# Performance work log

Measured on AMD Instinct MI355X. Metric: run time of the kernel, lower is better.

Reference implementation:

```python
import jax, jax.numpy as jnp
import numpy as np

WINDOW_SIZE = 100  # band half-width = WINDOW_SIZE // 2 = 50, inclusive


def setup_inputs() -> dict:
    key = jax.random.key(0)
    kq, kk, kv = jax.random.split(key, 3)
    shape = (2, 8, 4096, 64)  # [B, H, S, D]
    return {
        "query": jax.random.normal(kq, shape, dtype=jnp.float32),
        "key": jax.random.normal(kk, shape, dtype=jnp.float32),
        "value": jax.random.normal(kv, shape, dtype=jnp.float32),
    }


def reference(query, key, value):
    B, H, S, D = query.shape
    half = WINDOW_SIZE // 2
    scale = 1.0 / jnp.sqrt(jnp.asarray(D, dtype=jnp.float32))
    # Full dense scores (faithful to the original module): [B, H, S, S]
    scores = jnp.einsum("bhqd,bhkd->bhqk", query, key) * scale
    # Sliding-window band mask: row i attends to j in [i-half, i+half]
    idx = jnp.arange(S)
    band = jnp.abs(idx[:, None] - idx[None, :]) <= half  # [S, S]
    scores = jnp.where(band[None, None, :, :], scores, -jnp.inf)
    attn = jax.nn.softmax(scores, axis=-1)
    attn = jnp.nan_to_num(attn, nan=0.0)  # matches torch.nan_to_num(w, 0.0)
    return jnp.einsum("bhqk,bhkd->bhqd", attn, value)
```

## Files before the change

### kernel.cpp

```cpp
#include <hip/hip_runtime.h>

#define S_LEN 4096
#define DIM   64
#define HALF  50
#define RB    256
#define WQ    16
#define THREADS 1024
#define KCAP  384
#define SCALE 0.125f

typedef __attribute__((ext_vector_type(8))) short bf16x8;
typedef __attribute__((ext_vector_type(4))) float f32x4;

__device__ __forceinline__ unsigned int bf16_rne(float f) {
    unsigned int u = __float_as_uint(f);
    return (u + 0x7fffu + ((u >> 16) & 1u)) >> 16;
}
__device__ __forceinline__ unsigned int pk2(float lo, float hi) {
    return bf16_rne(lo) | (bf16_rne(hi) << 16);
}
__device__ __forceinline__ bf16x8 cvt8(float4 a, float4 b) {
    uint4 t = make_uint4(pk2(a.x, a.y), pk2(a.z, a.w), pk2(b.x, b.y), pk2(b.z, b.w));
    return __builtin_bit_cast(bf16x8, t);
}

__global__ __launch_bounds__(THREADS, 4)
void lattn_mfma(const float* __restrict__ Q, const float* __restrict__ K,
                const float* __restrict__ V, float* __restrict__ O) {
    __shared__ unsigned short Ks[KCAP * 64];
    __shared__ unsigned short Vs[DIM * KCAP];
    __shared__ unsigned short Ps[16 * 16 * 40];

    const int nwg = gridDim.x;
    const int cpx = nwg >> 3;
    const int bid = blockIdx.x;
    const int logical = (bid & 7) * cpx + (bid >> 3);
    const int bh = logical >> 4;
    const int r0 = (logical & 15) * RB;

    const size_t base = (size_t)bh * (S_LEN * DIM);
    const float* Qg = Q + base;
    const float* Kg = K + base;
    const float* Vg = V + base;
    float*       Og = O + base;

    const int kstart = (r0 >= HALF) ? ((r0 - HALF) & ~31) : 0;
    const int kend   = min(S_LEN, r0 + RB + HALF);

    const int u = threadIdx.x;
    const int lane = u & 63;
    const int wv_  = u >> 6;
    const int g  = lane >> 4;
    const int cc = lane & 15;
    const int qlo = r0 + WQ * wv_;

    float4 kA[3], kB[3];
    float4 vA[2][4];
    float4 qA[2], qB[2];

    #pragma unroll
    for (int i = 0; i < 3; ++i) {
        const int kg  = kstart + (u >> 3) + i * 128;
        const int oct = u & 7;
        if (kg < kend) {
            const float* p = Kg + (size_t)kg * DIM + oct * 8;
            kA[i] = *(const float4*)p; kB[i] = *(const float4*)(p + 4);
        } else {
            kA[i] = make_float4(0.f, 0.f, 0.f, 0.f); kB[i] = kA[i];
        }
    }
    #pragma unroll
    for (int i = 0; i < 2; ++i) {
        if (i == 0 || u < 512) {
            const int kg = kstart + (u >> 3) * 2 + i * 256;
            const int d0 = (u & 7) * 8;
            if (kg < kend) {
                const float* p = Vg + (size_t)kg * DIM + d0;
                vA[i][0] = *(const float4*)p;         vA[i][1] = *(const float4*)(p + 4);
                vA[i][2] = *(const float4*)(p + DIM); vA[i][3] = *(const float4*)(p + DIM + 4);
            } else {
                vA[i][0] = make_float4(0.f, 0.f, 0.f, 0.f);
                vA[i][1] = vA[i][0]; vA[i][2] = vA[i][0]; vA[i][3] = vA[i][0];
            }
        }
    }
    #pragma unroll
    for (int ds = 0; ds < 2; ++ds) {
        const float* src = Qg + (size_t)(qlo + cc) * DIM + ds * 32 + g * 8;
        qA[ds] = *(const float4*)src;
        qB[ds] = *(const float4*)(src + 4);
    }
    __builtin_amdgcn_sched_barrier(0);

    #pragma unroll
    for (int i = 0; i < 3; ++i) {
        const int krow = (u >> 3) + i * 128;
        const int oct  = u & 7;
        *(uint4*)(Ks + krow * 64 + ((oct ^ (krow & 7)) << 3)) =
            __builtin_bit_cast(uint4, cvt8(kA[i], kB[i]));
    }
    #pragma unroll
    for (int i = 0; i < 2; ++i) {
        if (i == 0 || u < 512) {
            const int k0 = (u >> 3) * 2 + i * 256;
            const int m  = u & 7;
            const float* a0 = (const float*)&vA[i][0];
            const float* a1 = (const float*)&vA[i][2];
            #pragma unroll
            for (int j = 0; j < 8; ++j) {
                const int d  = m * 8 + j;
                const int sl = (k0 >> 3) ^ j ^ m;
                *(unsigned int*)(Vs + d * KCAP + sl * 8 + (k0 & 7)) = pk2(a0[j], a1[j]);
            }
        }
    }
    bf16x8 qf[2];
    #pragma unroll
    for (int ds = 0; ds < 2; ++ds) {
        float4 a = qA[ds], b = qB[ds];
        a.x*=SCALE; a.y*=SCALE; a.z*=SCALE; a.w*=SCALE;
        b.x*=SCALE; b.y*=SCALE; b.z*=SCALE; b.w*=SCALE;
        qf[ds] = cvt8(a, b);
    }

    __syncthreads();

    f32x4 oacc[4] = {};
    float denom = 0.f;

    int lo = (qlo >= HALF) ? (qlo - HALF) : 0;
    lo = max(kstart, lo & ~31);
    const int t0 = (lo - kstart) >> 5;
    const int hi = min(kend, qlo + WQ - 1 + HALF + 1);
    const int t1 = (hi - kstart + 31) >> 5;

    unsigned short* Pw = Ps + wv_ * (16 * 40);

    for (int st = t0; st < t1; ++st) {
        const int kb32 = st << 5;

        f32x4 sacc[2] = {};
        #pragma unroll
        for (int ds = 0; ds < 2; ++ds) {
            #pragma unroll
            for (int kt = 0; kt < 2; ++kt) {
                const int krow = kb32 + kt * 16 + cc;
                const int sl   = (ds * 4 + g) ^ (krow & 7);
                const bf16x8 kfr = *(const bf16x8*)(Ks + krow * 64 + sl * 8);
                sacc[kt] = __builtin_amdgcn_mfma_f32_16x16x32_bf16(kfr, qf[ds], sacc[kt], 0, 0, 0);
            }
        }

        const int q = qlo + cc;
        #pragma unroll
        for (int kt = 0; kt < 2; ++kt) {
            float w4[4];
            const int keyb = kstart + kb32 + kt * 16 + g * 4;
            #pragma unroll
            for (int r = 0; r < 4; ++r) {
                const int key = keyb + r;
                const float e = __expf(fminf(sacc[kt][r], 60.f));
                const int dd  = key - q;
                const bool ok = (dd >= -HALF) && (dd <= HALF) && (key < S_LEN);
                w4[r] = ok ? e : 0.f;
                denom += w4[r];
            }
            *(uint2*)(Pw + cc * 40 + kt * 16 + g * 4) =
                make_uint2(pk2(w4[0], w4[1]), pk2(w4[2], w4[3]));
        }
        const bf16x8 pf = *(const bf16x8*)(Pw + cc * 40 + g * 8);

        #pragma unroll
        for (int dt = 0; dt < 4; ++dt) {
            const int d  = dt * 16 + cc;
            const int sl = ((kb32 >> 3) + g) ^ (d & 7) ^ ((d >> 3) & 7);
            const bf16x8 vf = *(const bf16x8*)(Vs + d * KCAP + sl * 8);
            oacc[dt] = __builtin_amdgcn_mfma_f32_16x16x32_bf16(vf, pf, oacc[dt], 0, 0, 0);
        }
    }

    denom += __shfl_xor(denom, 16);
    denom += __shfl_xor(denom, 32);
    const float rinv = 1.f / denom;
    float* dst = Og + (size_t)(qlo + cc) * DIM;
    #pragma unroll
    for (int dt = 0; dt < 4; ++dt) {
        const f32x4 o = oacc[dt];
        *(float4*)(dst + dt * 16 + g * 4) =
            make_float4(o[0] * rinv, o[1] * rinv, o[2] * rinv, o[3] * rinv);
    }
}

extern "C" void kernel_launch(void* const* d_in, const int* in_sizes, int n_in,
                              void* d_out, int out_size, void* d_ws, size_t ws_size,
                              hipStream_t stream) {
    const float* q = (const float*)d_in[0];
    const float* k = (const float*)d_in[1];
    const float* v = (const float*)d_in[2];
    float* o = (float*)d_out;
    const int nbh = in_sizes[0] / (S_LEN * DIM);
    dim3 grid((S_LEN / RB) * nbh);
    lattn_mfma<<<grid, THREADS, 0, stream>>>(q, k, v, o);
}
```

Before: 22.57 us.

## Stream K fragments directly from global with register prefetch, halve block size

Removes K staging in shared memory. Each wave now loads its K rows straight from global into registers, converts them to bf16 in registers, and prefetches the next 32-key tile while computing the current one. The block shrinks to 128 rows and 512 threads, so the grid doubles, and the main loop is fully unrolled to at most five tiles. This cuts LDS footprint and the cooperative K staging pass, in exchange for redundant global K reads across waves (overlapping bands) and more register pressure.

```diff
diff --git a/kernel.cpp b/kernel.cpp
--- a/kernel.cpp
+++ b/kernel.cpp
@@ -3,10 +3,11 @@
 #define S_LEN 4096
 #define DIM   64
 #define HALF  50
-#define RB    256
+#define RB    128
 #define WQ    16
-#define THREADS 1024
-#define KCAP  384
+#define THREADS 512
+#define KCAP  256
+#define NT    5
 #define SCALE 0.125f
 
 typedef __attribute__((ext_vector_type(8))) short bf16x8;
@@ -27,16 +28,15 @@
 __global__ __launch_bounds__(THREADS, 4)
 void lattn_mfma(const float* __restrict__ Q, const float* __restrict__ K,
                 const float* __restrict__ V, float* __restrict__ O) {
-    __shared__ unsigned short Ks[KCAP * 64];
     __shared__ unsigned short Vs[DIM * KCAP];
-    __shared__ unsigned short Ps[16 * 16 * 40];
+    __shared__ unsigned short Ps[8 * 16 * 40];
 
     const int nwg = gridDim.x;
     const int cpx = nwg >> 3;
     const int bid = blockIdx.x;
     const int logical = (bid & 7) * cpx + (bid >> 3);
-    const int bh = logical >> 4;
-    const int r0 = (logical & 15) * RB;
+    const int bh = logical >> 5;
+    const int r0 = (logical & 31) * RB;
 
     const size_t base = (size_t)bh * (S_LEN * DIM);
     const float* Qg = Q + base;
@@ -54,36 +54,22 @@
     const int cc = lane & 15;
     const int qlo = r0 + WQ * wv_;
 
-    float4 kA[3], kB[3];
     float4 vA[2][4];
+    #pragma unroll
+    for (int i = 0; i < 2; ++i) {
+        const int idx = u + i * THREADS;
+        const int kg  = kstart + (idx >> 3) * 2;
+        const int d0  = (idx & 7) * 8;
+        if (kg < kend) {
+            const float* p = Vg + (size_t)kg * DIM + d0;
+            vA[i][0] = *(const float4*)p;         vA[i][1] = *(const float4*)(p + 4);
+            vA[i][2] = *(const float4*)(p + DIM); vA[i][3] = *(const float4*)(p + DIM + 4);
+        } else {
+            vA[i][0] = make_float4(0.f, 0.f, 0.f, 0.f);
+            vA[i][1] = vA[i][0]; vA[i][2] = vA[i][0]; vA[i][3] = vA[i][0];
+        }
+    }
     float4 qA[2], qB[2];
-
-    #pragma unroll
-    for (int i = 0; i < 3; ++i) {
-        const int kg  = kstart + (u >> 3) + i * 128;
-        const int oct = u & 7;
-        if (kg < kend) {
-            const float* p = Kg + (size_t)kg * DIM + oct * 8;
-            kA[i] = *(const float4*)p; kB[i] = *(const float4*)(p + 4);
-        } else {
-            kA[i] = make_float4(0.f, 0.f, 0.f, 0.f); kB[i] = kA[i];
-        }
-    }
-    #pragma unroll
-    for (int i = 0; i < 2; ++i) {
-        if (i == 0 || u < 512) {
-            const int kg = kstart + (u >> 3) * 2 + i * 256;
-            const int d0 = (u & 7) * 8;
-            if (kg < kend) {
-                const float* p = Vg + (size_t)kg * DIM + d0;
-                vA[i][0] = *(const float4*)p;         vA[i][1] = *(const float4*)(p + 4);
-                vA[i][2] = *(const float4*)(p + DIM); vA[i][3] = *(const float4*)(p + DIM + 4);
-            } else {
-                vA[i][0] = make_float4(0.f, 0.f, 0.f, 0.f);
-                vA[i][1] = vA[i][0]; vA[i][2] = vA[i][0]; vA[i][3] = vA[i][0];
-            }
-        }
-    }
     #pragma unroll
     for (int ds = 0; ds < 2; ++ds) {
         const float* src = Qg + (size_t)(qlo + cc) * DIM + ds * 32 + g * 8;
@@ -93,25 +79,17 @@
     __builtin_amdgcn_sched_barrier(0);
 
     #pragma unroll
-    for (int i = 0; i < 3; ++i) {
-        const int krow = (u >> 3) + i * 128;
-        const int oct  = u & 7;
-        *(uint4*)(Ks + krow * 64 + ((oct ^ (krow & 7)) << 3)) =
-            __builtin_bit_cast(uint4, cvt8(kA[i], kB[i]));
-    }
-    #pragma unroll
     for (int i = 0; i < 2; ++i) {
-        if (i == 0 || u < 512) {
-            const int k0 = (u >> 3) * 2 + i * 256;
-            const int m  = u & 7;
-            const float* a0 = (const float*)&vA[i][0];
-            const float* a1 = (const float*)&vA[i][2];
-            #pragma unroll
-            for (int j = 0; j < 8; ++j) {
-                const int d  = m * 8 + j;
-                const int sl = (k0 >> 3) ^ j ^ m;
-                *(unsigned int*)(Vs + d * KCAP + sl * 8 + (k0 & 7)) = pk2(a0[j], a1[j]);
-            }
+        const int idx = u + i * THREADS;
+        const int k0  = (idx >> 3) * 2;
+        const int m   = idx & 7;
+        const float* a0 = (const float*)&vA[i][0];
+        const float* a1 = (const float*)&vA[i][2];
+        #pragma unroll
+        for (int j = 0; j < 8; ++j) {
+            const int d  = m * 8 + j;
+            const int sl = (k0 >> 3) ^ j ^ m;
+            *(unsigned int*)(Vs + d * KCAP + sl * 8 + (k0 & 7)) = pk2(a0[j], a1[j]);
         }
     }
     bf16x8 qf[2];
@@ -125,57 +103,83 @@
 
     __syncthreads();
 
-    f32x4 oacc[4] = {};
-    float denom = 0.f;
-
     int lo = (qlo >= HALF) ? (qlo - HALF) : 0;
     lo = max(kstart, lo & ~31);
     const int t0 = (lo - kstart) >> 5;
     const int hi = min(kend, qlo + WQ - 1 + HALF + 1);
     const int t1 = (hi - kstart + 31) >> 5;
 
-    unsigned short* Pw = Ps + wv_ * (16 * 40);
-
-    for (int st = t0; st < t1; ++st) {
+    float4 kraw[8];
+    auto k_issue = [&](int st) {
         const int kb32 = st << 5;
-
-        f32x4 sacc[2] = {};
-        #pragma unroll
-        for (int ds = 0; ds < 2; ++ds) {
-            #pragma unroll
-            for (int kt = 0; kt < 2; ++kt) {
-                const int krow = kb32 + kt * 16 + cc;
-                const int sl   = (ds * 4 + g) ^ (krow & 7);
-                const bf16x8 kfr = *(const bf16x8*)(Ks + krow * 64 + sl * 8);
-                sacc[kt] = __builtin_amdgcn_mfma_f32_16x16x32_bf16(kfr, qf[ds], sacc[kt], 0, 0, 0);
-            }
-        }
-
-        const int q = qlo + cc;
         #pragma unroll
         for (int kt = 0; kt < 2; ++kt) {
-            float w4[4];
-            const int keyb = kstart + kb32 + kt * 16 + g * 4;
-            #pragma unroll
-            for (int r = 0; r < 4; ++r) {
-                const int key = keyb + r;
-                const float e = __expf(fminf(sacc[kt][r], 60.f));
-                const int dd  = key - q;
-                const bool ok = (dd >= -HALF) && (dd <= HALF) && (key < S_LEN);
-                w4[r] = ok ? e : 0.f;
-                denom += w4[r];
-            }
-            *(uint2*)(Pw + cc * 40 + kt * 16 + g * 4) =
-                make_uint2(pk2(w4[0], w4[1]), pk2(w4[2], w4[3]));
-        }
-        const bf16x8 pf = *(const bf16x8*)(Pw + cc * 40 + g * 8);
-
-        #pragma unroll
-        for (int dt = 0; dt < 4; ++dt) {
-            const int d  = dt * 16 + cc;
-            const int sl = ((kb32 >> 3) + g) ^ (d & 7) ^ ((d >> 3) & 7);
-            const bf16x8 vf = *(const bf16x8*)(Vs + d * KCAP + sl * 8);
-            oacc[dt] = __builtin_amdgcn_mfma_f32_16x16x32_bf16(vf, pf, oacc[dt], 0, 0, 0);
+            const int krow = kstart + kb32 + kt * 16 + cc;
+            if (krow < kend) {
+                const float* p = Kg + (size_t)krow * DIM + g * 8;
+                kraw[kt*4+0] = *(const float4*)p;        kraw[kt*4+1] = *(const float4*)(p + 4);
+                kraw[kt*4+2] = *(const float4*)(p + 32); kraw[kt*4+3] = *(const float4*)(p + 36);
+            } else {
+                kraw[kt*4+0] = make_float4(0.f, 0.f, 0.f, 0.f);
+                kraw[kt*4+1] = kraw[kt*4+0]; kraw[kt*4+2] = kraw[kt*4+0]; kraw[kt*4+3] = kraw[kt*4+0];
+            }
+        }
+    };
+
+    unsigned short* Pw = Ps + wv_ * (16 * 40);
+    f32x4 oacc[4] = {};
+    float denom = 0.f;
+
+    k_issue(t0);
+
+    #pragma unroll
+    for (int i = 0; i < NT; ++i) {
+        const int st = t0 + i;
+        if (st < t1) {
+            const int kb32 = st << 5;
+
+            bf16x8 ka[2][2];
+            #pragma unroll
+            for (int kt = 0; kt < 2; ++kt) {
+                ka[0][kt] = cvt8(kraw[kt*4+0], kraw[kt*4+1]);
+                ka[1][kt] = cvt8(kraw[kt*4+2], kraw[kt*4+3]);
+            }
+            if (st + 1 < t1) k_issue(st + 1);
+
+            f32x4 sacc[2] = {};
+            #pragma unroll
+            for (int ds = 0; ds < 2; ++ds) {
+                #pragma unroll
+                for (int kt = 0; kt < 2; ++kt)
+                    sacc[kt] = __builtin_amdgcn_mfma_f32_16x16x32_bf16(ka[ds][kt], qf[ds], sacc[kt], 0, 0, 0);
+            }
+
+            const int q = qlo + cc;
+            #pragma unroll
+            for (int kt = 0; kt < 2; ++kt) {
+                float w4[4];
+                const int keyb = kstart + kb32 + kt * 16 + g * 4;
+                #pragma unroll
+                for (int r = 0; r < 4; ++r) {
+                    const int key = keyb + r;
+                    const float e = __expf(fminf(sacc[kt][r], 60.f));
+                    const int dd  = key - q;
+                    const bool ok = (dd >= -HALF) && (dd <= HALF) && (key < S_LEN);
+                    w4[r] = ok ? e : 0.f;
+                    denom += w4[r];
+                }
+                *(uint2*)(Pw + cc * 40 + kt * 16 + g * 4) =
+                    make_uint2(pk2(w4[0], w4[1]), pk2(w4[2], w4[3]));
+            }
+            const bf16x8 pf = *(const bf16x8*)(Pw + cc * 40 + g * 8);
+
+            #pragma unroll
+            for (int dt = 0; dt < 4; ++dt) {
+                const int d  = dt * 16 + cc;
+                const int sl = ((kb32 >> 3) + g) ^ (d & 7) ^ ((d >> 3) & 7);
+                const bf16x8 vf = *(const bf16x8*)(Vs + d * KCAP + sl * 8);
+                oacc[dt] = __builtin_amdgcn_mfma_f32_16x16x32_bf16(vf, pf, oacc[dt], 0, 0, 0);
+            }
         }
     }
 
```

Result: slower. 64.09 us (+183.9%).
